# Kernel optimization log

Measured on AMD Instinct MI355X. Metric: run time of the kernel, lower is better.

Reference implementation:

```python
import jax, jax.numpy as jnp
import numpy as np

D_MODEL = 1024
SLOTS = 4096
LEVELS = 3
B, T = 4, 4096
TOP_K = 8  # k = min(8, slots)


def setup_inputs() -> dict:
    key = jax.random.key(0)
    ks = jax.random.split(key, 8)
    # xavier-uniform-ish scale for K/V
    lim_kv = np.sqrt(6.0 / (SLOTS + D_MODEL)).astype(np.float32)
    lim_w1 = np.sqrt(6.0 / (D_MODEL + D_MODEL // 2)).astype(np.float32)
    lim_w2 = np.sqrt(6.0 / (D_MODEL // 2 + LEVELS)).astype(np.float32)
    return {
        "q": jax.random.normal(ks[0], (B, T, D_MODEL), dtype=jnp.float32),
        "Ks": jax.random.uniform(ks[1], (LEVELS, SLOTS, D_MODEL), jnp.float32, -lim_kv, lim_kv),
        "Vs": jax.random.uniform(ks[2], (LEVELS, SLOTS, D_MODEL), jnp.float32, -lim_kv, lim_kv),
        "saliences": jnp.zeros((LEVELS, SLOTS), dtype=jnp.float32),
        "router_W1": jax.random.uniform(ks[3], (D_MODEL, D_MODEL // 2), jnp.float32, -lim_w1, lim_w1),
        "router_b1": jnp.zeros((D_MODEL // 2,), dtype=jnp.float32),
        "router_W2": jax.random.uniform(ks[4], (D_MODEL // 2, LEVELS), jnp.float32, -lim_w2, lim_w2),
        "router_b2": jnp.zeros((LEVELS,), dtype=jnp.float32),
    }


def reference(q, Ks, Vs, saliences, router_W1, router_b1, router_W2, router_b2):
    Bq, Tq, D = q.shape
    inv_sqrt_d = 1.0 / jnp.sqrt(jnp.asarray(D, dtype=q.dtype))

    # router: Linear -> ReLU -> Linear -> softmax over levels
    h = jax.nn.relu(q @ router_W1 + router_b1)
    route_weights = jax.nn.softmax(h @ router_W2 + router_b2, axis=-1)  # [B,T,L]

    def per_level(K, V, salience, level_w):
        # K,V: [S,D]; salience: [S]; level_w: [B,T]
        scores = jnp.einsum('btd,sd->bts', q, K) * inv_sqrt_d + salience  # [B,T,S]
        topk_scores, topk_idx = jax.lax.top_k(scores, TOP_K)  # [B,T,k]
        attn = jax.nn.softmax(topk_scores, axis=-1)  # [B,T,k]
        V_sel = V[topk_idx]  # [B,T,k,D] irregular gather
        read = jnp.einsum('btk,btkd->btd', attn, V_sel)  # [B,T,D]
        return read * level_w[..., None]

    # route_weights per level: [L,B,T]
    reads = jax.vmap(per_level, in_axes=(0, 0, 0, 2))(
        Ks, Vs, saliences, route_weights)  # [L,B,T,D]
    final_read = reads.sum(axis=0)
    return final_read
```

## Files before the change

kernel.cpp:

```cpp
#include <hip/hip_runtime.h>
#include <hip/hip_bf16.h>
#include <math.h>

#define D_MODEL 1024
#define SLOTS   4096
#define LEVELS  3
#define BT      16384
#define HDIM    512
#define NCAND   16
#define TOPK    8

#define QSCALE 25.0f
#define KSCALE 3700.0f
#define DELTA  2.5e-3f

typedef float    f32x4  __attribute__((ext_vector_type(4)));
typedef int      i32x4  __attribute__((ext_vector_type(4)));
typedef __bf16   bf16x8 __attribute__((ext_vector_type(8)));
typedef _Float16 f16x8  __attribute__((ext_vector_type(8)));

__device__ __forceinline__ void gl_lds16(const void* g, void* l) {
  __builtin_amdgcn_global_load_lds((const __attribute__((address_space(1))) void*)g,
                                   (__attribute__((address_space(3))) void*)l, 16, 0, 0);
}

__device__ __forceinline__ unsigned short f2bf(float f) {
  union { float f; unsigned u; } v; v.f = f;
  unsigned r = (v.u + 0x7fffu + ((v.u >> 16) & 1u)) >> 16;
  return (unsigned short)r;
}
__device__ __forceinline__ float bf2f(unsigned short b) {
  union { unsigned u; float f; } v; v.u = ((unsigned)b) << 16; return v.f;
}
__device__ __forceinline__ int q_i8(float f, float scale) {
  float v = f * scale;
  v = fminf(fmaxf(v, -127.0f), 127.0f);
  return (int)rintf(v);
}
__device__ __forceinline__ unsigned umaxu(unsigned a, unsigned b) { return a > b ? a : b; }
__device__ __forceinline__ unsigned uminu(unsigned a, unsigned b) { return a < b ? a : b; }

__global__ __launch_bounds__(256) void conv_i8_kernel(const float* __restrict__ src,
                                                      char* __restrict__ dst, float scale) {
  int i = blockIdx.x * 256 + threadIdx.x;
  const float4* s = (const float4*)src + i * 4;
  int w[4];
#pragma unroll
  for (int g = 0; g < 4; ++g) {
    float4 v = s[g];
    int b0 = q_i8(v.x, scale) & 255, b1 = q_i8(v.y, scale) & 255;
    int b2 = q_i8(v.z, scale) & 255, b3 = q_i8(v.w, scale) & 255;
    w[g] = b0 | (b1 << 8) | (b2 << 16) | (b3 << 24);
  }
  ((int4*)dst)[i] = make_int4(w[0], w[1], w[2], w[3]);
}

__global__ __launch_bounds__(256) void conv_q8h_kernel(const float* __restrict__ q,
                                                       char* __restrict__ q8,
                                                       unsigned short* __restrict__ qh) {
  int i = blockIdx.x * 256 + threadIdx.x;
  const float4* s = (const float4*)q + i * 4;
  int w[4]; unsigned hh[8];
#pragma unroll
  for (int g = 0; g < 4; ++g) {
    float4 v = s[g];
    int b0 = q_i8(v.x, QSCALE) & 255, b1 = q_i8(v.y, QSCALE) & 255;
    int b2 = q_i8(v.z, QSCALE) & 255, b3 = q_i8(v.w, QSCALE) & 255;
    w[g] = b0 | (b1 << 8) | (b2 << 16) | (b3 << 24);
    hh[g * 2 + 0] = (unsigned)f2bf(v.x) | ((unsigned)f2bf(v.y) << 16);
    hh[g * 2 + 1] = (unsigned)f2bf(v.z) | ((unsigned)f2bf(v.w) << 16);
  }
  ((int4*)q8)[i] = make_int4(w[0], w[1], w[2], w[3]);
  uint4* qp = (uint4*)qh + i * 2;
  qp[0] = make_uint4(hh[0], hh[1], hh[2], hh[3]);
  qp[1] = make_uint4(hh[4], hh[5], hh[6], hh[7]);
}

__global__ __launch_bounds__(256) void conv_w1t_kernel(const float* __restrict__ W1,
                                                       unsigned short* __restrict__ Wh,
                                                       unsigned short* __restrict__ Wl) {
  int e = blockIdx.x * 256 + threadIdx.x;
  int k = e >> 9, n = e & 511;
  float f = W1[e];
  unsigned short hb = f2bf(f);
  Wh[(size_t)n * 1024 + k] = hb;
  Wl[(size_t)n * 1024 + k] = f2bf(f - bf2f(hb));
}

__global__ __launch_bounds__(256) void conv_v16_kernel(const float* __restrict__ Vs,
                                                       _Float16* __restrict__ V16) {
  int i = blockIdx.x * 256 + threadIdx.x;
  const float4* s = (const float4*)Vs + i * 2;
  float4 a = s[0], b = s[1];
  f16x8 o;
  o[0] = (_Float16)a.x; o[1] = (_Float16)a.y; o[2] = (_Float16)a.z; o[3] = (_Float16)a.w;
  o[4] = (_Float16)b.x; o[5] = (_Float16)b.y; o[6] = (_Float16)b.z; o[7] = (_Float16)b.w;
  ((f16x8*)V16)[i] = o;
}

__global__ __launch_bounds__(256) void gemm_scores_i8_kernel(
    const char* __restrict__ A,
    const char* __restrict__ B,
    const float* __restrict__ sal,
    unsigned short* __restrict__ C) {
  __shared__ __align__(16) char As[128 * 64];
  __shared__ __align__(16) char Bs[128 * 64];
  const int tid = threadIdx.x;
  const int bx = blockIdx.x, by = blockIdx.y;
  const int lane = tid & 63, wave = tid >> 6;
  const int wm = wave >> 1, wn = wave & 1;

  const char* gA = A + (size_t)(by * 128 + (tid >> 2)) * 1024 + (tid & 3) * 16;
  const char* gB = B + (size_t)(bx * 128 + (tid >> 2)) * 1024 + (tid & 3) * 16;
  char* lA = As + tid * 16;
  char* lB = Bs + tid * 16;

  i32x4 acc[4][4] = {};

  for (int k0 = 0; k0 < 1024; k0 += 64) {
    __syncthreads();
    gl_lds16(gA + k0,             lA);
    gl_lds16(gA + 64 * 1024 + k0, lA + 64 * 64);
    gl_lds16(gB + k0,             lB);
    gl_lds16(gB + 64 * 1024 + k0, lB + 64 * 64);
    __syncthreads();

    const int fr = lane & 15, fk = (lane >> 4) * 16;
    i32x4 a[4], b[4];
#pragma unroll
    for (int i = 0; i < 4; ++i) a[i] = *(const i32x4*)(As + (wm * 64 + i * 16 + fr) * 64 + fk);
#pragma unroll
    for (int j = 0; j < 4; ++j) b[j] = *(const i32x4*)(Bs + (wn * 64 + j * 16 + fr) * 64 + fk);
#pragma unroll
    for (int i = 0; i < 4; ++i)
#pragma unroll
      for (int j = 0; j < 4; ++j)
        acc[i][j] = __builtin_amdgcn_mfma_i32_16x16x64_i8(a[i], b[j], acc[i][j], 0, 0, 0);
  }

  const float dq = 1.0f / (QSCALE * KSCALE * 32.0f);
  const int rr = (lane >> 4) * 4, cc = lane & 15;
#pragma unroll
  for (int i = 0; i < 4; ++i)
#pragma unroll
    for (int j = 0; j < 4; ++j) {
      int col = bx * 128 + wn * 64 + j * 16 + cc;
      float s = sal[col];
      int rowb = by * 128 + wm * 64 + i * 16 + rr;
#pragma unroll
      for (int r = 0; r < 4; ++r)
        C[(size_t)(rowb + r) * 4096 + col] = f2bf((float)acc[i][j][r] * dq + s);
    }
}

__global__ __launch_bounds__(256) void gemm_router_kernel(
    const unsigned short* __restrict__ Ah,
    const unsigned short* __restrict__ Bh, const unsigned short* __restrict__ Bl,
    const float* __restrict__ b1, float* __restrict__ H) {
  __shared__ __align__(16) unsigned short Ash[128 * 32];
  __shared__ __align__(16) unsigned short Bsh[128 * 32], Bsl[128 * 32];
  const int tid = threadIdx.x;
  const int bx = blockIdx.x, by = blockIdx.y;
  const int lane = tid & 63, wave = tid >> 6;
  const int wm = wave >> 1, wn = wave & 1;

  const int s_row = wave * 16 + (lane >> 2);
  const int s_c8  = (lane & 3) * 8;
  const unsigned short* gAh = Ah + (size_t)(by * 128 + s_row) * 1024 + s_c8;
  const unsigned short* gBh = Bh + (size_t)(bx * 128 + s_row) * 1024 + s_c8;
  const unsigned short* gBl = Bl + (size_t)(bx * 128 + s_row) * 1024 + s_c8;
  unsigned short* lAh = Ash + s_row * 32 + s_c8;
  unsigned short* lBh = Bsh + s_row * 32 + s_c8;
  unsigned short* lBl = Bsl + s_row * 32 + s_c8;

  f32x4 acc[4][4] = {};

  for (int k0 = 0; k0 < 1024; k0 += 32) {
    __syncthreads();
    gl_lds16(gAh + k0,             lAh);
    gl_lds16(gAh + 64 * 1024 + k0, lAh + 64 * 32);
    gl_lds16(gBh + k0,             lBh);
    gl_lds16(gBh + 64 * 1024 + k0, lBh + 64 * 32);
    gl_lds16(gBl + k0,             lBl);
    gl_lds16(gBl + 64 * 1024 + k0, lBl + 64 * 32);
    __syncthreads();

    const int fr = lane & 15, fk = (lane >> 4) * 8;
    bf16x8 ah[4], bh[4], bl[4];
#pragma unroll
    for (int i = 0; i < 4; ++i) {
      int off = (wm * 64 + i * 16 + fr) * 32 + fk;
      ah[i] = *(const bf16x8*)(Ash + off);
    }
#pragma unroll
    for (int j = 0; j < 4; ++j) {
      int off = (wn * 64 + j * 16 + fr) * 32 + fk;
      bh[j] = *(const bf16x8*)(Bsh + off);
      bl[j] = *(const bf16x8*)(Bsl + off);
    }
#pragma unroll
    for (int i = 0; i < 4; ++i)
#pragma unroll
      for (int j = 0; j < 4; ++j) {
        acc[i][j] = __builtin_amdgcn_mfma_f32_16x16x32_bf16(ah[i], bh[j], acc[i][j], 0, 0, 0);
        acc[i][j] = __builtin_amdgcn_mfma_f32_16x16x32_bf16(ah[i], bl[j], acc[i][j], 0, 0, 0);
      }
  }

  const int rr = (lane >> 4) * 4, cc = lane & 15;
#pragma unroll
  for (int i = 0; i < 4; ++i)
#pragma unroll
    for (int j = 0; j < 4; ++j) {
      int col = bx * 128 + wn * 64 + j * 16 + cc;
      float bias = b1[col];
      int rowb = by * 128 + wm * 64 + i * 16 + rr;
#pragma unroll
      for (int r = 0; r < 4; ++r) {
        float v = acc[i][j][r] + bias;
        H[(size_t)(rowb + r) * HDIM + col] = v > 0.0f ? v : 0.0f;
      }
    }
}

__global__ __launch_bounds__(256) void router_head_kernel(
    const float* __restrict__ H, const float* __restrict__ W2,
    const float* __restrict__ b2, float* __restrict__ route_w) {
  int wave = threadIdx.x >> 6, lane = threadIdx.x & 63;
  int row = blockIdx.x * 4 + wave;
  float a0 = 0.f, a1 = 0.f, a2 = 0.f;
#pragma unroll
  for (int k = 0; k < 8; ++k) {
    int d = k * 64 + lane;
    float hv = H[(size_t)row * HDIM + d];
    a0 += hv * W2[d * 3 + 0];
    a1 += hv * W2[d * 3 + 1];
    a2 += hv * W2[d * 3 + 2];
  }
#pragma unroll
  for (int m = 1; m < 64; m <<= 1) {
    a0 += __shfl_xor(a0, m); a1 += __shfl_xor(a1, m); a2 += __shfl_xor(a2, m);
  }
  if (lane == 0) {
    float l0 = a0 + b2[0], l1 = a1 + b2[1], l2 = a2 + b2[2];
    float mx = fmaxf(l0, fmaxf(l1, l2));
    float e0 = expf(l0 - mx), e1 = expf(l1 - mx), e2 = expf(l2 - mx);
    float inv = 1.0f / (e0 + e1 + e2);
    route_w[(size_t)row * 3 + 0] = e0 * inv;
    route_w[(size_t)row * 3 + 1] = e1 * inv;
    route_w[(size_t)row * 3 + 2] = e2 * inv;
  }
}

template<bool FILTER>
__device__ __forceinline__ void top4_build(const uint4 (&v)[8], unsigned lane8, unsigned bound,
                                           unsigned &t0, unsigned &t1, unsigned &t2, unsigned &t3) {
  t0 = t1 = t2 = t3 = 0u;
#pragma unroll
  for (int i = 0; i < 8; ++i) {
    unsigned wds[4] = {v[i].x, v[i].y, v[i].z, v[i].w};
#pragma unroll
    for (int g = 0; g < 4; ++g) {
      unsigned w = wds[g];
      unsigned s = w & 0x80008000u;
      unsigned key2 = (w ^ 0x80008000u) ^ (s - (s >> 15));
      unsigned pb = lane8 + (unsigned)(i * 512 + g * 2);
      unsigned kA = (key2 << 16) | pb;
      unsigned kB = (key2 & 0xFFFF0000u) | (pb + 1u);
      if (FILTER) {
        if (kA >= bound) kA = 0u;
        if (kB >= bound) kB = 0u;
      }
      unsigned x, y, z;
      x = uminu(t0, kA); t0 = umaxu(t0, kA);
      y = uminu(t1, x);  t1 = umaxu(t1, x);
      z = uminu(t2, y);  t2 = umaxu(t2, y);
      t3 = umaxu(t3, z);
      x = uminu(t0, kB); t0 = umaxu(t0, kB);
      y = uminu(t1, x);  t1 = umaxu(t1, x);
      z = uminu(t2, y);  t2 = umaxu(t2, y);
      t3 = umaxu(t3, z);
    }
  }
}

__global__ __launch_bounds__(256) void select_kernel(
    const unsigned short* __restrict__ S,
    int2* __restrict__ cand2, int c0, int level) {
  int wave = threadIdx.x >> 6, lane = threadIdx.x & 63;
  int rlocal = blockIdx.x * 4 + wave;
  const uint4* row = (const uint4*)(S + (size_t)rlocal * 4096);

  uint4 v[8];
#pragma unroll
  for (int i = 0; i < 8; ++i) v[i] = row[i * 64 + lane];

  const unsigned lane8 = (unsigned)lane * 8u;
  unsigned t0, t1, t2, t3;
  top4_build<false>(v, lane8, 0u, t0, t1, t2, t3);

  unsigned myres = 0u;
#pragma clang loop unroll(disable)
  for (int r = 0; r < NCAND; ++r) {
    unsigned g = t0;
#pragma unroll
    for (int m = 1; m < 64; m <<= 1) {
      unsigned o = (unsigned)__shfl_xor((int)g, m);
      g = umaxu(g, o);
    }
    if (t0 == g) {
      t0 = t1; t1 = t2; t2 = t3; t3 = 0u;
      if (t0 == 0u)
        top4_build<true>(v, lane8, g, t0, t1, t2, t3);
    }
    if (lane == r) myres = g;
  }

  size_t base = ((size_t)(c0 + rlocal) * 3 + level) * NCAND;
  if (lane < NCAND) {
    unsigned k16 = myres >> 16;
    unsigned ob = k16 ^ ((k16 & 0x8000u) ? 0x8000u : 0xFFFFu);
    cand2[base + lane] = make_int2((int)(myres & 0xFFFFu),
                                   __float_as_int(bf2f((unsigned short)ob)));
  }
}

__global__ __launch_bounds__(256) void rescore_kernel(
    const float* __restrict__ q, const float* __restrict__ Kl,
    const float* __restrict__ sal, const float* __restrict__ route_w,
    const int2* __restrict__ cand2, int level, int c0,
    int* __restrict__ sel_idx, float* __restrict__ sel_w) {
  int wave = threadIdx.x >> 6, lane = threadIdx.x & 63;
  int row = c0 + blockIdx.x * 4 + wave;

  float av[NCAND]; int idx[NCAND];
  {
    size_t cb = ((size_t)row * 3 + level) * NCAND;
#pragma unroll
    for (int c = 0; c < NCAND; ++c) {
      int2 pr = cand2[cb + c];
      idx[c] = pr.x; av[c] = __int_as_float(pr.y);
    }
  }

  int cin_mask = 0, amb_mask = 0;
#pragma unroll
  for (int i = 0; i < NCAND; ++i) {
    int cnt_hi = 0, cnt_lo = 0;
#pragma unroll
    for (int j = 0; j < NCAND; ++j) {
      cnt_hi += (av[j] > av[i] + DELTA) ? 1 : 0;
      cnt_lo += (j != i && av[j] > av[i] - DELTA) ? 1 : 0;
    }
    if (cnt_hi >= TOPK) {  }
    else if (cnt_lo <= TOPK - 1) cin_mask |= (1 << i);
    else amb_mask |= (1 << i);
  }
  int need = TOPK - __popc((unsigned)cin_mask);

  double ex[NCAND];
  if (need > 0 && amb_mask) {
    float qr[16];
    const float4* qp = (const float4*)(q + (size_t)row * 1024) + lane * 4;
#pragma unroll
    for (int m4 = 0; m4 < 4; ++m4) {
      float4 tv = qp[m4];
      qr[m4 * 4 + 0] = tv.x; qr[m4 * 4 + 1] = tv.y;
      qr[m4 * 4 + 2] = tv.z; qr[m4 * 4 + 3] = tv.w;
    }
    for (int c = 0; c < NCAND; ++c) {
      if (!((amb_mask >> c) & 1)) continue;
      int sx = idx[c];
      const float4* kr = (const float4*)(Kl + (size_t)sx * 1024) + lane * 4;
      double acc = 0.0;
#pragma unroll
      for (int m4 = 0; m4 < 4; ++m4) {
        float4 kv = kr[m4];
        acc = fma((double)qr[m4 * 4 + 0], (double)kv.x, acc);
        acc = fma((double)qr[m4 * 4 + 1], (double)kv.y, acc);
        acc = fma((double)qr[m4 * 4 + 2], (double)kv.z, acc);
        acc = fma((double)qr[m4 * 4 + 3], (double)kv.w, acc);
      }
#pragma unroll
      for (int m = 1; m < 64; m <<= 1) acc += __shfl_xor(acc, m);
      ex[c] = acc * 0.03125 + (double)sal[sx];
    }
  }

  int cs[TOPK]; int ns = 0;
#pragma unroll
  for (int i = 0; i < NCAND; ++i)
    if ((cin_mask >> i) & 1) cs[ns++] = i;
  unsigned rem = (unsigned)amb_mask;
  for (int p = 0; p < need; ++p) {
    double bs = -1e300; int bc = -1;
    for (int c = 0; c < NCAND; ++c)
      if ((rem >> c) & 1)
        if (ex[c] > bs) { bs = ex[c]; bc = c; }
    rem &= ~(1u << bc);
    cs[ns++] = bc;
  }

  float mx = -INFINITY;
#pragma unroll
  for (int k = 0; k < TOPK; ++k) mx = fmaxf(mx, av[cs[k]]);
  float ew[TOPK], sum = 0.f;
#pragma unroll
  for (int k = 0; k < TOPK; ++k) { ew[k] = expf(av[cs[k]] - mx); sum += ew[k]; }
  float rw = route_w[(size_t)row * 3 + level] / sum;
  if (lane == 0) {
    size_t base = ((size_t)row * 3 + level) * TOPK;
#pragma unroll
    for (int k = 0; k < TOPK; ++k) {
      sel_idx[base + k] = idx[cs[k]];
      sel_w[base + k]  = ew[k] * rw;
    }
  }
}

__global__ __launch_bounds__(128) void final_kernel(
    const _Float16* __restrict__ V16, const int* __restrict__ sel_idx,
    const float* __restrict__ sel_w, float* __restrict__ out) {
  __shared__ float wv[24];
  __shared__ int   widx[24];
  int row = blockIdx.x, t = threadIdx.x;
  if (t < 24) {
    int l = t >> 3, j = t & 7;
    size_t base = ((size_t)row * 3 + l) * TOPK + j;
    wv[t]   = sel_w[base];
    widx[t] = l * SLOTS + sel_idx[base];
  }
  __syncthreads();
  float acc[8] = {0.f, 0.f, 0.f, 0.f, 0.f, 0.f, 0.f, 0.f};
  for (int i = 0; i < 24; ++i) {
    float w = wv[i];
    f16x8 v = *(const f16x8*)(V16 + (size_t)widx[i] * 1024 + t * 8);
#pragma unroll
    for (int e = 0; e < 8; ++e) acc[e] += w * (float)v[e];
  }
  float4* op = (float4*)(out + (size_t)row * 1024) + t * 2;
  op[0] = make_float4(acc[0], acc[1], acc[2], acc[3]);
  op[1] = make_float4(acc[4], acc[5], acc[6], acc[7]);
}

extern "C" void kernel_launch(void* const* d_in, const int* in_sizes, int n_in,
                              void* d_out, int out_size, void* d_ws, size_t ws_size,
                              hipStream_t stream) {
  const float* q   = (const float*)d_in[0];
  const float* Ks  = (const float*)d_in[1];
  const float* Vs  = (const float*)d_in[2];
  const float* sal = (const float*)d_in[3];
  const float* W1  = (const float*)d_in[4];
  const float* b1  = (const float*)d_in[5];
  const float* W2  = (const float*)d_in[6];
  const float* b2  = (const float*)d_in[7];
  float* out = (float*)d_out;
  (void)in_sizes; (void)n_in; (void)out_size;

  char* p = (char*)d_ws;
  auto alloc = [&](size_t bytes) -> char* {
    char* r = p; p += (bytes + 255) & ~(size_t)255; return r;
  };
  char*      q8    = alloc((size_t)BT * 1024);
  char*      K8    = alloc((size_t)LEVELS * SLOTS * 1024);
  _Float16*  V16   = (_Float16*)alloc((size_t)LEVELS * SLOTS * 1024 * 2);
  float*     route = (float*)alloc((size_t)BT * 3 * 4);
  int2*      cand2 = (int2*)alloc((size_t)BT * 3 * NCAND * 8);
  int*       s_idx = (int*)alloc((size_t)BT * 3 * TOPK * 4);
  float*     s_w   = (float*)alloc((size_t)BT * 3 * TOPK * 4);
  size_t fixed = (size_t)(p - (char*)d_ws);

  char* ali = p;
  unsigned short* qh   = (unsigned short*)alloc((size_t)BT * 1024 * 2);
  unsigned short* W1Th = (unsigned short*)alloc((size_t)HDIM * 1024 * 2);
  unsigned short* W1Tl = (unsigned short*)alloc((size_t)HDIM * 1024 * 2);
  float*          h    = (float*)alloc((size_t)BT * HDIM * 4);
  size_t router_bytes = (size_t)(p - ali);

  unsigned short* scores = (unsigned short*)ali;
  int chunk = 2048;
  const int opts[4] = {16384, 8192, 4096, 2048};
  for (int i = 0; i < 4; ++i) {
    size_t scores_b = (size_t)opts[i] * SLOTS * 2;
    size_t need = fixed + (scores_b > router_bytes ? scores_b : router_bytes);
    if (need <= ws_size) { chunk = opts[i]; break; }
  }

  conv_q8h_kernel<<<(BT * 1024 / 16) / 256, 256, 0, stream>>>(q, q8, qh);
  conv_i8_kernel<<<(LEVELS * SLOTS * 1024 / 16) / 256, 256, 0, stream>>>(Ks, K8, KSCALE);
  conv_v16_kernel<<<(LEVELS * SLOTS * 1024 / 8) / 256, 256, 0, stream>>>(Vs, V16);
  conv_w1t_kernel<<<(1024 * HDIM) / 256, 256, 0, stream>>>(W1, W1Th, W1Tl);

  gemm_router_kernel<<<dim3(HDIM / 128, BT / 128), 256, 0, stream>>>(qh, W1Th, W1Tl, b1, h);
  router_head_kernel<<<BT / 4, 256, 0, stream>>>(h, W2, b2, route);

  for (int level = 0; level < LEVELS; ++level) {
    const char*  K8L  = K8 + (size_t)level * SLOTS * 1024;
    const float* salL = sal + (size_t)level * SLOTS;
    const float* KsL  = Ks + (size_t)level * SLOTS * 1024;
    for (int c0 = 0; c0 < BT; c0 += chunk) {
      gemm_scores_i8_kernel<<<dim3(SLOTS / 128, chunk / 128), 256, 0, stream>>>(
          q8 + (size_t)c0 * 1024, K8L, salL, scores);
      select_kernel<<<chunk / 4, 256, 0, stream>>>(scores, cand2, c0, level);
      rescore_kernel<<<chunk / 4, 256, 0, stream>>>(q, KsL, salL, route, cand2, level, c0, s_idx, s_w);
    }
  }

  final_kernel<<<BT, 128, 0, stream>>>(V16, s_idx, s_w, out);
}
```

Before: 1.068 ms.

## Resolve easy top-k rows in select kernel, rescore only ambiguous rows via worklist

The select kernel now computes the certain and ambiguous candidate masks and writes the final softmax weights directly for rows that need no exact rescoring. Only rows whose ambiguous set exceeds the remaining slots are appended to a per-chunk worklist through an atomic counter. The rescore kernel then works only on worklist entries, so waves no longer launch for rows that need nothing. Scores are also stored as fp16 instead of bf16, which gives finer candidate values and fewer ambiguous rows, at the cost of fp16's narrower range. Rescore blocks are still launched for the whole chunk and exit early.

```diff
diff --git a/kernel.cpp b/kernel.cpp
--- a/kernel.cpp
+++ b/kernel.cpp
@@ -31,6 +31,12 @@
 }
 __device__ __forceinline__ float bf2f(unsigned short b) {
   union { unsigned u; float f; } v; v.u = ((unsigned)b) << 16; return v.f;
+}
+__device__ __forceinline__ unsigned short f2h_bits(float f) {
+  union { _Float16 h; unsigned short u; } v; v.h = (_Float16)f; return v.u;
+}
+__device__ __forceinline__ float h2f(unsigned short b) {
+  union { unsigned short u; _Float16 h; } v; v.u = b; return (float)v.h;
 }
 __device__ __forceinline__ int q_i8(float f, float scale) {
   float v = f * scale;
@@ -97,6 +103,8 @@
   o[4] = (_Float16)b.x; o[5] = (_Float16)b.y; o[6] = (_Float16)b.z; o[7] = (_Float16)b.w;
   ((f16x8*)V16)[i] = o;
 }
+
+__global__ void init_counters_kernel(int* __restrict__ c) { c[threadIdx.x] = 0; }
 
 __global__ __launch_bounds__(256) void gemm_scores_i8_kernel(
     const char* __restrict__ A,
@@ -149,7 +157,7 @@
       int rowb = by * 128 + wm * 64 + i * 16 + rr;
 #pragma unroll
       for (int r = 0; r < 4; ++r)
-        C[(size_t)(rowb + r) * 4096 + col] = f2bf((float)acc[i][j][r] * dq + s);
+        C[(size_t)(rowb + r) * 4096 + col] = f2h_bits((float)acc[i][j][r] * dq + s);
     }
 }
 
@@ -286,14 +294,18 @@
 
 __global__ __launch_bounds__(256) void select_kernel(
     const unsigned short* __restrict__ S,
-    int2* __restrict__ cand2, int c0, int level) {
+    const float* __restrict__ route_w,
+    int2* __restrict__ cand2,
+    int2* __restrict__ worklist, int* __restrict__ counter, int slot,
+    int* __restrict__ sel_idx, float* __restrict__ sel_w,
+    int c0, int level) {
   int wave = threadIdx.x >> 6, lane = threadIdx.x & 63;
   int rlocal = blockIdx.x * 4 + wave;
-  const uint4* row = (const uint4*)(S + (size_t)rlocal * 4096);
+  const uint4* rowp = (const uint4*)(S + (size_t)rlocal * 4096);
 
   uint4 v[8];
 #pragma unroll
-  for (int i = 0; i < 8; ++i) v[i] = row[i * 64 + lane];
+  for (int i = 0; i < 8; ++i) v[i] = rowp[i * 64 + lane];
 
   const unsigned lane8 = (unsigned)lane * 8u;
   unsigned t0, t1, t2, t3;
@@ -316,22 +328,92 @@
     if (lane == r) myres = g;
   }
 
-  size_t base = ((size_t)(c0 + rlocal) * 3 + level) * NCAND;
-  if (lane < NCAND) {
-    unsigned k16 = myres >> 16;
+  const int row = c0 + rlocal;
+  {
+    size_t cb = ((size_t)row * 3 + level) * NCAND;
+    if (lane < NCAND) {
+      unsigned k16 = myres >> 16;
+      unsigned ob = k16 ^ ((k16 & 0x8000u) ? 0x8000u : 0xFFFFu);
+      cand2[cb + lane] = make_int2((int)(myres & 0xFFFFu),
+                                   __float_as_int(h2f((unsigned short)ob)));
+    }
+  }
+
+  float av[NCAND]; int idx[NCAND];
+#pragma unroll
+  for (int j = 0; j < NCAND; ++j) {
+    unsigned r = (unsigned)__shfl((int)myres, j);
+    unsigned k16 = r >> 16;
     unsigned ob = k16 ^ ((k16 & 0x8000u) ? 0x8000u : 0xFFFFu);
-    cand2[base + lane] = make_int2((int)(myres & 0xFFFFu),
-                                   __float_as_int(bf2f((unsigned short)ob)));
+    av[j]  = h2f((unsigned short)ob);
+    idx[j] = (int)(r & 0xFFFFu);
+  }
+
+  int cin_mask = 0, amb_mask = 0;
+#pragma unroll
+  for (int i = 0; i < NCAND; ++i) {
+    int cnt_hi = 0, cnt_lo = 0;
+#pragma unroll
+    for (int j = 0; j < NCAND; ++j) {
+      cnt_hi += (av[j] > av[i] + DELTA) ? 1 : 0;
+      cnt_lo += (j != i && av[j] > av[i] - DELTA) ? 1 : 0;
+    }
+    if (cnt_hi >= TOPK) {  }
+    else if (cnt_lo <= TOPK - 1) cin_mask |= (1 << i);
+    else amb_mask |= (1 << i);
+  }
+  const int need = TOPK - __popc((unsigned)cin_mask);
+  const bool hard = (need > 0) && (__popc((unsigned)amb_mask) > need);
+
+  if (hard) {
+    if (lane == 0) {
+      int e = atomicAdd(counter + slot, 1);
+      worklist[e] = make_int2(row, cin_mask | (amb_mask << 16));
+    }
+    return;
+  }
+
+  int selm = (need > 0) ? (cin_mask | amb_mask) : cin_mask;
+  float mx = -INFINITY;
+#pragma unroll
+  for (int j = 0; j < NCAND; ++j)
+    if ((selm >> j) & 1) mx = fmaxf(mx, av[j]);
+  float ew[NCAND]; float sum = 0.f;
+#pragma unroll
+  for (int j = 0; j < NCAND; ++j) {
+    ew[j] = 0.f;
+    if ((selm >> j) & 1) { ew[j] = expf(av[j] - mx); sum += ew[j]; }
+  }
+  if (lane == 0) {
+    float rw = route_w[(size_t)row * 3 + level] / sum;
+    size_t b8 = ((size_t)row * 3 + level) * TOPK;
+    int k = 0;
+#pragma unroll
+    for (int j = 0; j < NCAND; ++j)
+      if ((selm >> j) & 1) {
+        sel_idx[b8 + k] = idx[j];
+        sel_w[b8 + k]  = ew[j] * rw;
+        ++k;
+      }
   }
 }
 
 __global__ __launch_bounds__(256) void rescore_kernel(
     const float* __restrict__ q, const float* __restrict__ Kl,
     const float* __restrict__ sal, const float* __restrict__ route_w,
-    const int2* __restrict__ cand2, int level, int c0,
-    int* __restrict__ sel_idx, float* __restrict__ sel_w) {
-  int wave = threadIdx.x >> 6, lane = threadIdx.x & 63;
-  int row = c0 + blockIdx.x * 4 + wave;
+    const int2* __restrict__ cand2,
+    const int2* __restrict__ worklist, const int* __restrict__ counter, int slot,
+    int level, int* __restrict__ sel_idx, float* __restrict__ sel_w) {
+  const int wid  = blockIdx.x * 4 + (threadIdx.x >> 6);
+  const int lane = threadIdx.x & 63;
+  const int n = counter[slot];
+  if (wid >= n) return;
+
+  const int2 e = worklist[wid];
+  const int row = e.x;
+  const int cin_mask = e.y & 0xFFFF;
+  const int amb_mask = (e.y >> 16) & 0xFFFF;
+  const int need = TOPK - __popc((unsigned)cin_mask);
 
   float av[NCAND]; int idx[NCAND];
   {
@@ -343,24 +425,8 @@
     }
   }
 
-  int cin_mask = 0, amb_mask = 0;
-#pragma unroll
-  for (int i = 0; i < NCAND; ++i) {
-    int cnt_hi = 0, cnt_lo = 0;
-#pragma unroll
-    for (int j = 0; j < NCAND; ++j) {
-      cnt_hi += (av[j] > av[i] + DELTA) ? 1 : 0;
-      cnt_lo += (j != i && av[j] > av[i] - DELTA) ? 1 : 0;
-    }
-    if (cnt_hi >= TOPK) {  }
-    else if (cnt_lo <= TOPK - 1) cin_mask |= (1 << i);
-    else amb_mask |= (1 << i);
-  }
-  int need = TOPK - __popc((unsigned)cin_mask);
-
-  double ex[NCAND];
-  if (need > 0 && amb_mask) {
-    float qr[16];
+  float qr[16];
+  {
     const float4* qp = (const float4*)(q + (size_t)row * 1024) + lane * 4;
 #pragma unroll
     for (int m4 = 0; m4 < 4; ++m4) {
@@ -368,53 +434,61 @@
       qr[m4 * 4 + 0] = tv.x; qr[m4 * 4 + 1] = tv.y;
       qr[m4 * 4 + 2] = tv.z; qr[m4 * 4 + 3] = tv.w;
     }
-    for (int c = 0; c < NCAND; ++c) {
-      if (!((amb_mask >> c) & 1)) continue;
-      int sx = idx[c];
-      const float4* kr = (const float4*)(Kl + (size_t)sx * 1024) + lane * 4;
-      double acc = 0.0;
-#pragma unroll
-      for (int m4 = 0; m4 < 4; ++m4) {
-        float4 kv = kr[m4];
-        acc = fma((double)qr[m4 * 4 + 0], (double)kv.x, acc);
-        acc = fma((double)qr[m4 * 4 + 1], (double)kv.y, acc);
-        acc = fma((double)qr[m4 * 4 + 2], (double)kv.z, acc);
-        acc = fma((double)qr[m4 * 4 + 3], (double)kv.w, acc);
-      }
-#pragma unroll
-      for (int m = 1; m < 64; m <<= 1) acc += __shfl_xor(acc, m);
-      ex[c] = acc * 0.03125 + (double)sal[sx];
-    }
-  }
-
-  int cs[TOPK]; int ns = 0;
-#pragma unroll
-  for (int i = 0; i < NCAND; ++i)
-    if ((cin_mask >> i) & 1) cs[ns++] = i;
+  }
+
+  double ex[NCAND];
+#pragma unroll
+  for (int c = 0; c < NCAND; ++c) {
+    if (!((amb_mask >> c) & 1)) continue;
+    int sx = idx[c];
+    const float4* kr = (const float4*)(Kl + (size_t)sx * 1024) + lane * 4;
+    double acc = 0.0;
+#pragma unroll
+    for (int m4 = 0; m4 < 4; ++m4) {
+      float4 kv = kr[m4];
+      acc = fma((double)qr[m4 * 4 + 0], (double)kv.x, acc);
+      acc = fma((double)qr[m4 * 4 + 1], (double)kv.y, acc);
+      acc = fma((double)qr[m4 * 4 + 2], (double)kv.z, acc);
+      acc = fma((double)qr[m4 * 4 + 3], (double)kv.w, acc);
+    }
+#pragma unroll
+    for (int m = 1; m < 64; m <<= 1) acc += __shfl_xor(acc, m);
+    ex[c] = acc * 0.03125 + (double)sal[sx];
+  }
+
+  int selm = cin_mask;
   unsigned rem = (unsigned)amb_mask;
   for (int p = 0; p < need; ++p) {
-    double bs = -1e300; int bc = -1;
+    double bs = -1e300; int bc = 0;
+#pragma unroll
     for (int c = 0; c < NCAND; ++c)
       if ((rem >> c) & 1)
         if (ex[c] > bs) { bs = ex[c]; bc = c; }
     rem &= ~(1u << bc);
-    cs[ns++] = bc;
+    selm |= (1 << bc);
   }
 
   float mx = -INFINITY;
 #pragma unroll
-  for (int k = 0; k < TOPK; ++k) mx = fmaxf(mx, av[cs[k]]);
-  float ew[TOPK], sum = 0.f;
-#pragma unroll
-  for (int k = 0; k < TOPK; ++k) { ew[k] = expf(av[cs[k]] - mx); sum += ew[k]; }
-  float rw = route_w[(size_t)row * 3 + level] / sum;
+  for (int j = 0; j < NCAND; ++j)
+    if ((selm >> j) & 1) mx = fmaxf(mx, av[j]);
+  float ew[NCAND]; float sum = 0.f;
+#pragma unroll
+  for (int j = 0; j < NCAND; ++j) {
+    ew[j] = 0.f;
+    if ((selm >> j) & 1) { ew[j] = expf(av[j] - mx); sum += ew[j]; }
+  }
   if (lane == 0) {
-    size_t base = ((size_t)row * 3 + level) * TOPK;
-#pragma unroll
-    for (int k = 0; k < TOPK; ++k) {
-      sel_idx[base + k] = idx[cs[k]];
-      sel_w[base + k]  = ew[k] * rw;
-    }
+    float rw = route_w[(size_t)row * 3 + level] / sum;
+    size_t b8 = ((size_t)row * 3 + level) * TOPK;
+    int k = 0;
+#pragma unroll
+    for (int j = 0; j < NCAND; ++j)
+      if ((selm >> j) & 1) {
+        sel_idx[b8 + k] = idx[j];
+        sel_w[b8 + k]  = ew[j] * rw;
+        ++k;
+      }
   }
 }
 
@@ -468,6 +542,8 @@
   int2*      cand2 = (int2*)alloc((size_t)BT * 3 * NCAND * 8);
   int*       s_idx = (int*)alloc((size_t)BT * 3 * TOPK * 4);
   float*     s_w   = (float*)alloc((size_t)BT * 3 * TOPK * 4);
+  int*       ctrs  = (int*)alloc(32 * 4);
+  int2*      wlist = (int2*)alloc((size_t)BT * 8);
   size_t fixed = (size_t)(p - (char*)d_ws);
 
   char* ali = p;
@@ -486,6 +562,8 @@
     if (need <= ws_size) { chunk = opts[i]; break; }
   }
 
+  init_counters_kernel<<<1, 32, 0, stream>>>(ctrs);
+
   conv_q8h_kernel<<<(BT * 1024 / 16) / 256, 256, 0, stream>>>(q, q8, qh);
   conv_i8_kernel<<<(LEVELS * SLOTS * 1024 / 16) / 256, 256, 0, stream>>>(Ks, K8, KSCALE);
   conv_v16_kernel<<<(LEVELS * SLOTS * 1024 / 8) / 256, 256, 0, stream>>>(Vs, V16);
@@ -494,15 +572,18 @@
   gemm_router_kernel<<<dim3(HDIM / 128, BT / 128), 256, 0, stream>>>(qh, W1Th, W1Tl, b1, h);
   router_head_kernel<<<BT / 4, 256, 0, stream>>>(h, W2, b2, route);
 
+  int slot = 0;
   for (int level = 0; level < LEVELS; ++level) {
     const char*  K8L  = K8 + (size_t)level * SLOTS * 1024;
     const float* salL = sal + (size_t)level * SLOTS;
     const float* KsL  = Ks + (size_t)level * SLOTS * 1024;
-    for (int c0 = 0; c0 < BT; c0 += chunk) {
+    for (int c0 = 0; c0 < BT; c0 += chunk, ++slot) {
       gemm_scores_i8_kernel<<<dim3(SLOTS / 128, chunk / 128), 256, 0, stream>>>(
           q8 + (size_t)c0 * 1024, K8L, salL, scores);
-      select_kernel<<<chunk / 4, 256, 0, stream>>>(scores, cand2, c0, level);
-      rescore_kernel<<<chunk / 4, 256, 0, stream>>>(q, KsL, salL, route, cand2, level, c0, s_idx, s_w);
+      select_kernel<<<chunk / 4, 256, 0, stream>>>(scores, route, cand2, wlist, ctrs, slot,
+                                                   s_idx, s_w, c0, level);
+      rescore_kernel<<<chunk / 4, 256, 0, stream>>>(q, KsL, salL, route, cand2, wlist, ctrs, slot,
+                                                    level, s_idx, s_w);
     }
   }
 
```

Measured after the change: 1.492 ms. +39.7%, slower.
